# Performance work log

Hardware: AMD Instinct MI355X
Metric: run time of the kernel (lower is better)

## Reference

```python
import jax, jax.numpy as jnp
import numpy as np

N = 100000   # nodes
E = 3200000  # edges
D = 16       # n_qubits / feature dim
H = 64       # classifier hidden
C = 10       # output_dims
L = 2        # len(q_depths)


def setup_inputs() -> dict:
    key = jax.random.key(0)
    ks = jax.random.split(key, 16)
    s = 1.0 / np.sqrt(D)
    return {
        "x": jax.random.normal(ks[0], (N, D), jnp.float32),
        "edge_index": jax.random.randint(ks[1], (2, E), 0, N, dtype=jnp.int32),
        "edge_attr": jax.random.uniform(ks[2], (E,), jnp.float32),
        "batch": jnp.zeros((N,), jnp.int32),
        # per-layer GCNConv params
        "lin_w": jax.random.uniform(ks[3], (L, D, D), jnp.float32, -s, s),
        "conv_b": jnp.zeros((L, D), jnp.float32),
        # per-layer nodeNN (stand-in for quantum_net): tanh(W x + b)
        "node_w": jax.random.uniform(ks[4], (L, D, D), jnp.float32, -s, s),
        "node_b": jnp.zeros((L, D), jnp.float32),
        # per-layer LayerNorm affine
        "ln_g": jnp.ones((L, D), jnp.float32),
        "ln_b": jnp.zeros((L, D), jnp.float32),
        # classifier
        "w1": jax.random.normal(ks[5], (H, D), jnp.float32) * np.sqrt(2.0 / (D + H)),
        "b1": jnp.zeros((H,), jnp.float32),
        "w2": jax.random.normal(ks[6], (C, H), jnp.float32) * np.sqrt(2.0 / (H + C)),
        "b2": jnp.zeros((C,), jnp.float32),
    }


def _layer_norm(h, g, b, eps=1e-5):
    mu = h.mean(-1, keepdims=True)
    var = ((h - mu) ** 2).mean(-1, keepdims=True)
    return (h - mu) * jax.lax.rsqrt(var + eps) * g + b


def reference(x, edge_index, edge_attr, batch, lin_w, conv_b, node_w, node_b,
              ln_g, ln_b, w1, b1, w2, b2):
    n = x.shape[0]
    # gcn_norm with add_self_loops=True (fill_value=1)
    loop = jnp.arange(n, dtype=edge_index.dtype)
    row = jnp.concatenate([edge_index[0], loop])  # source
    col = jnp.concatenate([edge_index[1], loop])  # target
    ew = jnp.concatenate([edge_attr, jnp.ones((n,), x.dtype)])
    deg = jax.ops.segment_sum(ew, col, num_segments=n)
    dinv = jnp.where(deg > 0, jax.lax.rsqrt(jnp.maximum(deg, 1e-30)), 0.0)
    norm = dinv[row] * ew * dinv[col]  # [E+N]

    h = x
    n_layers = lin_w.shape[0]
    for i in range(n_layers):
        out = h @ lin_w[i].T                      # lin (no bias)
        msg = norm[:, None] * out[row]            # gather + scale, [E+N, D]
        agg = jax.ops.segment_sum(msg, col, num_segments=n)  # scatter-add
        out = jnp.tanh(agg @ node_w[i].T + node_b[i])  # nodeNN update (quantum_net stand-in)
        out = out + conv_b[i]
        h = jnp.where(out > 0, out, 0.2 * out)    # LeakyReLU(0.2)
        h = _layer_norm(h, ln_g[i], ln_b[i])

    h = jax.nn.relu(h @ w1.T + b1)                # classifier (dropout = identity at eval)
    return h @ w2.T + b2
```

## Files before the change

kernel.cpp:

```cpp
#include <hip/hip_runtime.h>
#include <hip/hip_bf16.h>

namespace {

constexpr int N_NODES = 100000;
constexpr int N_EDGES = 3200000;
constexpr int D = 16;
constexpr int H = 64;
constexpr int C = 10;
constexpr int L = 2;
constexpr int BLK = 256;
constexpr int BLKS = 512;
constexpr int NBN = (N_NODES + BLK - 1) / BLK;

constexpr int PA = 32;
constexpr int NP = (N_NODES + PA - 1) / PA;

constexpr int CBN = 256;
constexpr int NC = (N_NODES + CBN - 1) / CBN;
constexpr int NPTR = NC * CBN + 1;

constexpr int NBB = 1024;
constexpr int EC = N_EDGES / NBB;
constexpr int REC2_CAP = N_EDGES + 7 * N_NODES;

__device__ inline unsigned short f2bf(float f) {
  unsigned u = __float_as_uint(f);
  return (unsigned short)((u + 0x7FFFu + ((u >> 16) & 1u)) >> 16);
}
__device__ inline float bf2f(unsigned short b) {
  return __uint_as_float(((unsigned)b) << 16);
}

__global__ void k_bincount(const int* __restrict__ col, int* __restrict__ blk_hist) {
  __shared__ int lh[NC];
  for (int i = threadIdx.x; i < NC; i += BLKS) lh[i] = 0;
  __syncthreads();
  const int b = blockIdx.x;
  const int e0 = b * EC, e1 = e0 + EC;
  for (int e = e0 + threadIdx.x; e < e1; e += 4 * BLKS) {
    int cc[4]; bool ok[4];
#pragma unroll
    for (int j = 0; j < 4; ++j) {
      int ee = e + j * BLKS;
      ok[j] = ee < e1;
      cc[j] = ok[j] ? col[ee] : 0;
    }
#pragma unroll
    for (int j = 0; j < 4; ++j)
      if (ok[j]) atomicAdd(&lh[cc[j] >> 8], 1);
  }
  __syncthreads();
  for (int i = threadIdx.x; i < NC; i += BLKS)
    blk_hist[(size_t)b * NC + i] = lh[i];
}

__global__ void k_colscan(int* __restrict__ blk_hist, int* __restrict__ bin_cnt) {
  const int i = blockIdx.x;
  const int t = threadIdx.x;
  int v[4];
  int s = 0;
#pragma unroll
  for (int j = 0; j < 4; ++j) {
    v[j] = blk_hist[(size_t)(t * 4 + j) * NC + i];
    s += v[j];
  }
  const int lane = t & 63;
  int incl = s;
#pragma unroll
  for (int off = 1; off < 64; off <<= 1) {
    int y = __shfl_up(incl, off, 64);
    if (lane >= off) incl += y;
  }
  __shared__ int wsum[4];
  const int w = t >> 6;
  if (lane == 63) wsum[w] = incl;
  __syncthreads();
  int wbase = 0;
#pragma unroll
  for (int k = 0; k < 4; ++k) wbase += (k < w) ? wsum[k] : 0;
  int excl = wbase + incl - s;
#pragma unroll
  for (int j = 0; j < 4; ++j) {
    blk_hist[(size_t)(t * 4 + j) * NC + i] = excl;
    excl += v[j];
  }
  if (t == BLK - 1) bin_cnt[i] = excl;
}

__global__ void k_scan(const int* __restrict__ src, int* __restrict__ dst, int n,
                       int sentinel) {
  __shared__ int s0[2048], s1[2048];
  const int t = threadIdx.x;
  int v0 = (t < n) ? src[t] : 0;
  int v1 = (t + 1024 < n) ? src[t + 1024] : 0;
  s0[t] = v0; s0[t + 1024] = v1;
  __syncthreads();
  int* cur = s0; int* nxt = s1;
  for (int off = 1; off < 2048; off <<= 1) {
    nxt[t] = cur[t] + (t >= off ? cur[t - off] : 0);
    int i1 = t + 1024;
    nxt[i1] = cur[i1] + (i1 >= off ? cur[i1 - off] : 0);
    __syncthreads();
    int* tmp = cur; cur = nxt; nxt = tmp;
  }
  if (t < n) dst[t] = cur[t] - v0;
  if (t + 1024 < n) dst[t + 1024] = cur[t + 1024] - v1;
  if (t == 0 && sentinel >= 0) dst[n] = sentinel;
}

__global__ void k_binscatter(const int* __restrict__ row, const int* __restrict__ col,
                             const float* __restrict__ ew, const int* __restrict__ coarse_ptr,
                             const int* __restrict__ blk_hist, uint2* __restrict__ recs) {
  __shared__ int lcur[NC];
  const int b = blockIdx.x;
  for (int i = threadIdx.x; i < NC; i += BLKS)
    lcur[i] = coarse_ptr[i] + blk_hist[(size_t)b * NC + i];
  __syncthreads();
  const int e0 = b * EC, e1 = e0 + EC;
  for (int e = e0 + threadIdx.x; e < e1; e += 8 * BLKS) {
    int cc[8], rr[8]; float ww[8]; bool ok[8];
#pragma unroll
    for (int j = 0; j < 8; ++j) {
      int ee = e + j * BLKS;
      ok[j] = ee < e1;
      cc[j] = ok[j] ? col[ee] : 0;
      rr[j] = ok[j] ? row[ee] : 0;
      ww[j] = ok[j] ? ew[ee] : 0.f;
    }
#pragma unroll
    for (int j = 0; j < 8; ++j) {
      if (ok[j]) {
        int c = cc[j];
        int pos = atomicAdd(&lcur[c >> 8], 1);
        recs[pos] = make_uint2((unsigned)rr[j] | ((unsigned)(c & (CBN - 1)) << 17),
                               __float_as_uint(ww[j]));
      }
    }
  }
}

__global__ void k_cntnode(const uint2* __restrict__ recs, const int* __restrict__ coarse_ptr,
                          int* __restrict__ cnt_g, int* __restrict__ pad_cnt) {
  __shared__ int cnt[CBN];
  __shared__ int ws[4];
  const int b = blockIdx.x;
  const int tid = threadIdx.x;
  if (tid < CBN) cnt[tid] = 0;
  __syncthreads();
  const int beg = coarse_ptr[b], end = coarse_ptr[b + 1];
  for (int p = beg + tid; p < end; p += 4 * BLKS) {
    unsigned xx[4]; bool ok[4];
#pragma unroll
    for (int j = 0; j < 4; ++j) {
      int pp = p + j * BLKS;
      ok[j] = pp < end;
      xx[j] = ok[j] ? recs[pp].x : 0u;
    }
#pragma unroll
    for (int j = 0; j < 4; ++j)
      if (ok[j]) atomicAdd(&cnt[xx[j] >> 17], 1);
  }
  __syncthreads();
  if (tid < CBN) {
    int c = cnt[tid];
    cnt_g[b * CBN + tid] = c;
    int pv = (c + 7) & ~7;
#pragma unroll
    for (int m = 1; m < 64; m <<= 1) pv += __shfl_xor(pv, m, 64);
    if ((tid & 63) == 0) ws[tid >> 6] = pv;
  }
  __syncthreads();
  if (tid == 0) pad_cnt[b] = ws[0] + ws[1] + ws[2] + ws[3];
}

__global__ void k_sortscatter(const uint2* __restrict__ recs, const int* __restrict__ coarse_ptr,
                              const int* __restrict__ cnt_g, const int* __restrict__ pad_ptr,
                              int* __restrict__ node_ptr, uint2* __restrict__ recs2) {
  __shared__ int cur[CBN];
  __shared__ int fin[CBN];
  __shared__ int wsum[4];
  const int b = blockIdx.x;
  const int tid = threadIdx.x;
  int pc = 0, incl = 0;
  if (tid < CBN) {
    pc = (cnt_g[b * CBN + tid] + 7) & ~7;
    incl = pc;
    const int lane = tid & 63;
#pragma unroll
    for (int off = 1; off < 64; off <<= 1) {
      int y = __shfl_up(incl, off, 64);
      if (lane >= off) incl += y;
    }
    if (lane == 63) wsum[tid >> 6] = incl;
  }
  __syncthreads();
  if (tid < CBN) {
    const int w = tid >> 6;
    int wb = 0;
#pragma unroll
    for (int k = 0; k < 4; ++k) wb += (k < w) ? wsum[k] : 0;
    int excl = wb + incl - pc + pad_ptr[b];
    cur[tid] = excl;
    fin[tid] = excl + pc;
    node_ptr[b * CBN + tid] = excl;
    if (b == NC - 1 && tid == CBN - 1) node_ptr[NC * CBN] = excl + pc;
  }
  __syncthreads();
  const int beg = coarse_ptr[b], end = coarse_ptr[b + 1];
  for (int p = beg + tid; p < end; p += 4 * BLKS) {
    uint2 r[4]; bool ok[4];
#pragma unroll
    for (int j = 0; j < 4; ++j) {
      int pp = p + j * BLKS;
      ok[j] = pp < end;
      r[j] = ok[j] ? recs[pp] : make_uint2(0u, 0u);
    }
#pragma unroll
    for (int j = 0; j < 4; ++j) {
      if (ok[j]) {
        int pos = atomicAdd(&cur[r[j].x >> 17], 1);
        recs2[pos] = make_uint2(r[j].x & 0x1FFFF, r[j].y);
      }
    }
  }
  __syncthreads();
  if (tid < CBN) {
    for (int q = cur[tid]; q < fin[tid]; ++q) recs2[q] = make_uint2(0u, 0u);
  }
}

__global__ void k_dinv2(const int* __restrict__ node_ptr, const uint2* __restrict__ recs2,
                        float* __restrict__ dinv) {
  int v = blockIdx.x * BLK + threadIdx.x;
  if (v >= N_NODES) return;
  float s = 1.0f;
  int e = node_ptr[v + 1];
  for (int p = node_ptr[v]; p < e; ++p) s += __uint_as_float(recs2[p].y);
  dinv[v] = s > 0.f ? rsqrtf(fmaxf(s, 1e-30f)) : 0.f;
}

__global__ void k_lin(const float* __restrict__ hin, const float* __restrict__ W,
                      const float* __restrict__ dinv, unsigned short* __restrict__ outd) {
  __shared__ float sW[D * D];
  sW[threadIdx.x] = W[threadIdx.x];
  __syncthreads();
  int v = blockIdx.x * BLK + threadIdx.x;
  if (v >= N_NODES) return;
  float hv[D];
  const float4* hp = reinterpret_cast<const float4*>(hin + (size_t)v * D);
#pragma unroll
  for (int c = 0; c < 4; ++c) {
    float4 t = hp[c];
    hv[4 * c + 0] = t.x; hv[4 * c + 1] = t.y;
    hv[4 * c + 2] = t.z; hv[4 * c + 3] = t.w;
  }
  float dv = dinv[v];
  unsigned short ob[D];
#pragma unroll
  for (int j = 0; j < D; ++j) {
    float s = 0.f;
#pragma unroll
    for (int k = 0; k < D; ++k) s += hv[k] * sW[j * D + k];
    ob[j] = f2bf(s * dv);
  }
  uint4 w0, w1;
  w0.x = (unsigned)ob[0]  | ((unsigned)ob[1]  << 16);
  w0.y = (unsigned)ob[2]  | ((unsigned)ob[3]  << 16);
  w0.z = (unsigned)ob[4]  | ((unsigned)ob[5]  << 16);
  w0.w = (unsigned)ob[6]  | ((unsigned)ob[7]  << 16);
  w1.x = (unsigned)ob[8]  | ((unsigned)ob[9]  << 16);
  w1.y = (unsigned)ob[10] | ((unsigned)ob[11] << 16);
  w1.z = (unsigned)ob[12] | ((unsigned)ob[13] << 16);
  w1.w = (unsigned)ob[14] | ((unsigned)ob[15] << 16);
  uint4* op = reinterpret_cast<uint4*>(outd + (size_t)v * D);
  op[0] = w0;
  op[1] = w1;
}

__global__ void k_agg(const int* __restrict__ node_ptr, const uint2* __restrict__ recs2,
                      const float* __restrict__ dinv, const unsigned short* __restrict__ outd,
                      const float* __restrict__ Wn, const float* __restrict__ nb,
                      const float* __restrict__ cb, const float* __restrict__ lg,
                      const float* __restrict__ lb, float* __restrict__ h) {
  __shared__ float sacc[PA * 17];
  __shared__ float sdinv[PA];
  __shared__ float sWT[D * D];
  __shared__ float snb[D], scb[D], slg[D], slb[D];
  const int b = blockIdx.x;
  const int base = b * PA;
  const int tid = threadIdx.x;

  sWT[tid] = Wn[(tid & 15) * D + (tid >> 4)];
  if (tid < D) {
    snb[tid] = nb[tid]; scb[tid] = cb[tid];
    slg[tid] = lg[tid]; slb[tid] = lb[tid];
  }
  if (tid < PA) {
    int v = base + tid;
    sdinv[tid] = (v < N_NODES) ? dinv[v] : 0.f;
  }

  const int g = tid >> 4;
  const int l = tid & 15;
#pragma unroll
  for (int i = 0; i < PA / 16; ++i) {
    const int n = g + 16 * i;
    const int v = base + n;
    float acc = (v < N_NODES) ? bf2f(outd[(size_t)v * D + l]) : 0.f;
    int p = node_ptr[v];
    const int e = node_ptr[v + 1];
    uint4 a0, a1, a2, a3;
    if (p < e) {
      const uint4* rp = reinterpret_cast<const uint4*>(recs2 + p);
      a0 = rp[0]; a1 = rp[1]; a2 = rp[2]; a3 = rp[3];
    }
    for (; p < e; p += 8) {
      const int pn = (p + 8 < e) ? p + 8 : p;
      const uint4* rpn = reinterpret_cast<const uint4*>(recs2 + pn);
      uint4 b0 = rpn[0], b1 = rpn[1], b2 = rpn[2], b3 = rpn[3];
      float g0 = bf2f(outd[(size_t)a0.x * D + l]);
      float g1 = bf2f(outd[(size_t)a0.z * D + l]);
      float g2 = bf2f(outd[(size_t)a1.x * D + l]);
      float g3 = bf2f(outd[(size_t)a1.z * D + l]);
      float g4 = bf2f(outd[(size_t)a2.x * D + l]);
      float g5 = bf2f(outd[(size_t)a2.z * D + l]);
      float g6 = bf2f(outd[(size_t)a3.x * D + l]);
      float g7 = bf2f(outd[(size_t)a3.z * D + l]);
      acc = fmaf(__uint_as_float(a0.y), g0, acc);
      acc = fmaf(__uint_as_float(a0.w), g1, acc);
      acc = fmaf(__uint_as_float(a1.y), g2, acc);
      acc = fmaf(__uint_as_float(a1.w), g3, acc);
      acc = fmaf(__uint_as_float(a2.y), g4, acc);
      acc = fmaf(__uint_as_float(a2.w), g5, acc);
      acc = fmaf(__uint_as_float(a3.y), g6, acc);
      acc = fmaf(__uint_as_float(a3.w), g7, acc);
      a0 = b0; a1 = b1; a2 = b2; a3 = b3;
    }
    sacc[n * 17 + l] = acc;
  }
  __syncthreads();

#pragma unroll
  for (int nb0 = 0; nb0 < PA / 16; ++nb0) {
    int n = nb0 * 16 + g;
    int v = base + n;
    float s = 0.f;
#pragma unroll
    for (int k = 0; k < D; ++k) s += sacc[n * 17 + k] * sWT[k * D + l];
    s = snb[l] + sdinv[n] * s;
    float u = tanhf(s) + scb[l];
    u = u > 0.f ? u : 0.2f * u;
    float mu = u;
#pragma unroll
    for (int m = 1; m < 16; m <<= 1) mu += __shfl_xor(mu, m, 64);
    mu *= (1.0f / D);
    float dd = u - mu;
    float var = dd * dd;
#pragma unroll
    for (int m = 1; m < 16; m <<= 1) var += __shfl_xor(var, m, 64);
    var *= (1.0f / D);
    float inv = rsqrtf(var + 1e-5f);
    if (v < N_NODES) h[(size_t)v * D + l] = dd * inv * slg[l] + slb[l];
  }
}

__global__ void k_cls(const float* __restrict__ h, const float* __restrict__ w1,
                      const float* __restrict__ b1, const float* __restrict__ w2,
                      const float* __restrict__ b2, float* __restrict__ out) {
  __shared__ float sw1[H * D];
  __shared__ float sb1[H];
  __shared__ float sw2[C * H];
  __shared__ float sb2[C];
  for (int i = threadIdx.x; i < H * D; i += BLK) sw1[i] = w1[i];
  for (int i = threadIdx.x; i < H; i += BLK) sb1[i] = b1[i];
  for (int i = threadIdx.x; i < C * H; i += BLK) sw2[i] = w2[i];
  for (int i = threadIdx.x; i < C; i += BLK) sb2[i] = b2[i];
  __syncthreads();
  int v = blockIdx.x * BLK + threadIdx.x;
  if (v >= N_NODES) return;
  float hv[D];
  const float4* hp = reinterpret_cast<const float4*>(h + (size_t)v * D);
#pragma unroll
  for (int c = 0; c < 4; ++c) {
    float4 t = hp[c];
    hv[4 * c + 0] = t.x; hv[4 * c + 1] = t.y;
    hv[4 * c + 2] = t.z; hv[4 * c + 3] = t.w;
  }
  float oc[C];
#pragma unroll
  for (int c = 0; c < C; ++c) oc[c] = sb2[c];
#pragma unroll
  for (int j = 0; j < H; ++j) {
    float s = sb1[j];
#pragma unroll
    for (int k = 0; k < D; ++k) s += hv[k] * sw1[j * D + k];
    s = fmaxf(s, 0.f);
#pragma unroll
    for (int c = 0; c < C; ++c) oc[c] += s * sw2[c * H + j];
  }
#pragma unroll
  for (int c = 0; c < C; ++c) out[(size_t)v * C + c] = oc[c];
}

inline char* align_up(char* p, size_t a) {
  return (char*)(((uintptr_t)p + a - 1) & ~(uintptr_t)(a - 1));
}

}

extern "C" void kernel_launch(void* const* d_in, const int* in_sizes, int n_in,
                              void* d_out, int out_size, void* d_ws, size_t ws_size,
                              hipStream_t stream) {
  const float* x         = (const float*)d_in[0];
  const int*   edge_idx  = (const int*)d_in[1];
  const float* edge_attr = (const float*)d_in[2];
  const float* lin_w  = (const float*)d_in[4];
  const float* conv_b = (const float*)d_in[5];
  const float* node_w = (const float*)d_in[6];
  const float* node_b = (const float*)d_in[7];
  const float* ln_g   = (const float*)d_in[8];
  const float* ln_b   = (const float*)d_in[9];
  const float* w1     = (const float*)d_in[10];
  const float* b1     = (const float*)d_in[11];
  const float* w2     = (const float*)d_in[12];
  const float* b2     = (const float*)d_in[13];
  float* out = (float*)d_out;

  const int* row = edge_idx;
  const int* col = edge_idx + N_EDGES;

  char* p = (char*)d_ws;
  int*   bin_cnt    = (int*)p;   p = align_up(p + sizeof(int) * NC, 256);
  int*   coarse_ptr = (int*)p;   p = align_up(p + sizeof(int) * (NC + 1), 256);
  int*   pad_cnt    = (int*)p;   p = align_up(p + sizeof(int) * NC, 256);
  int*   pad_ptr    = (int*)p;   p = align_up(p + sizeof(int) * (NC + 1), 256);
  int*   cnt_g      = (int*)p;   p = align_up(p + sizeof(int) * (size_t)(NC * CBN), 256);
  int*   node_ptr   = (int*)p;   p = align_up(p + sizeof(int) * (size_t)NPTR, 256);
  float* dinv       = (float*)p; p = align_up(p + sizeof(float) * N_NODES, 256);
  char*  recs_mem   = p;         p = align_up(p + sizeof(uint2) * (size_t)N_EDGES, 256);
  uint2* recs2      = (uint2*)p; p = align_up(p + sizeof(uint2) * (size_t)REC2_CAP, 256);

  uint2* recs = (uint2*)recs_mem;
  unsigned short* outb = (unsigned short*)recs_mem;
  float* hbuf = (float*)align_up(recs_mem + sizeof(unsigned short) * (size_t)N_NODES * D, 256);
  int*   blk_hist = (int*)recs2;

  k_bincount<<<NBB, BLKS, 0, stream>>>(col, blk_hist);
  k_colscan<<<NC, BLK, 0, stream>>>(blk_hist, bin_cnt);
  k_scan<<<1, 1024, 0, stream>>>(bin_cnt, coarse_ptr, NC, N_EDGES);
  k_binscatter<<<NBB, BLKS, 0, stream>>>(row, col, edge_attr, coarse_ptr, blk_hist, recs);
  k_cntnode<<<NC, BLKS, 0, stream>>>(recs, coarse_ptr, cnt_g, pad_cnt);
  k_scan<<<1, 1024, 0, stream>>>(pad_cnt, pad_ptr, NC, -1);
  k_sortscatter<<<NC, BLKS, 0, stream>>>(recs, coarse_ptr, cnt_g, pad_ptr, node_ptr, recs2);
  k_dinv2<<<NBN, BLK, 0, stream>>>(node_ptr, recs2, dinv);

  for (int i = 0; i < L; ++i) {
    const float* hin = (i == 0) ? x : hbuf;
    k_lin<<<NBN, BLK, 0, stream>>>(hin, lin_w + i * D * D, dinv, outb);
    k_agg<<<NP, BLK, 0, stream>>>(node_ptr, recs2, dinv, outb,
                                  node_w + i * D * D, node_b + i * D, conv_b + i * D,
                                  ln_g + i * D, ln_b + i * D, hbuf);
  }
  k_cls<<<NBN, BLK, 0, stream>>>(hbuf, w1, b1, w2, b2, out);
}
```

Before: 194.5 us.

## Fuse next-layer linear and classifier into aggregation kernel epilogues

Measured after the change: 192.7 us. About the same (-0.9%).

```diff
diff --git a/kernel.cpp b/kernel.cpp
--- a/kernel.cpp
+++ b/kernel.cpp
@@ -8,7 +8,6 @@
 constexpr int D = 16;
 constexpr int H = 64;
 constexpr int C = 10;
-constexpr int L = 2;
 constexpr int BLK = 256;
 constexpr int BLKS = 512;
 constexpr int NBN = (N_NODES + BLK - 1) / BLK;
@@ -278,15 +277,26 @@
   op[1] = w1;
 }
 
+template <int MODE>
 __global__ void k_agg(const int* __restrict__ node_ptr, const uint2* __restrict__ recs2,
                       const float* __restrict__ dinv, const unsigned short* __restrict__ outd,
                       const float* __restrict__ Wn, const float* __restrict__ nb,
                       const float* __restrict__ cb, const float* __restrict__ lg,
-                      const float* __restrict__ lb, float* __restrict__ h) {
+                      const float* __restrict__ lb,
+                      const float* __restrict__ Wlin_next,
+                      unsigned short* __restrict__ outd_next,
+                      const float* __restrict__ w1, const float* __restrict__ b1,
+                      const float* __restrict__ w2, const float* __restrict__ b2,
+                      float* __restrict__ outc) {
   __shared__ float sacc[PA * 17];
   __shared__ float sdinv[PA];
   __shared__ float sWT[D * D];
   __shared__ float snb[D], scb[D], slg[D], slb[D];
+  __shared__ float sWT2[D * D];
+  __shared__ float sw1[H * D];
+  __shared__ float sb1[H];
+  __shared__ float sw2[C * H];
+  __shared__ float sb2[C];
   const int b = blockIdx.x;
   const int base = b * PA;
   const int tid = threadIdx.x;
@@ -296,10 +306,20 @@
     snb[tid] = nb[tid]; scb[tid] = cb[tid];
     slg[tid] = lg[tid]; slb[tid] = lb[tid];
   }
+  if constexpr (MODE == 1) {
+    sWT2[tid] = Wlin_next[(tid & 15) * D + (tid >> 4)];
+  }
+  if constexpr (MODE == 2) {
+    for (int i = tid; i < H * D; i += BLK) sw1[i] = w1[i];
+    if (tid < H) sb1[tid] = b1[tid];
+    for (int i = tid; i < C * H; i += BLK) sw2[i] = w2[i];
+    if (tid < C) sb2[tid] = b2[tid];
+  }
   if (tid < PA) {
     int v = base + tid;
     sdinv[tid] = (v < N_NODES) ? dinv[v] : 0.f;
   }
+  __syncthreads();
 
   const int g = tid >> 4;
   const int l = tid & 15;
@@ -318,7 +338,7 @@
     for (; p < e; p += 8) {
       const int pn = (p + 8 < e) ? p + 8 : p;
       const uint4* rpn = reinterpret_cast<const uint4*>(recs2 + pn);
-      uint4 b0 = rpn[0], b1 = rpn[1], b2 = rpn[2], b3 = rpn[3];
+      uint4 b0 = rpn[0], b1_ = rpn[1], b2_ = rpn[2], b3 = rpn[3];
       float g0 = bf2f(outd[(size_t)a0.x * D + l]);
       float g1 = bf2f(outd[(size_t)a0.z * D + l]);
       float g2 = bf2f(outd[(size_t)a1.x * D + l]);
@@ -335,7 +355,7 @@
       acc = fmaf(__uint_as_float(a2.w), g5, acc);
       acc = fmaf(__uint_as_float(a3.y), g6, acc);
       acc = fmaf(__uint_as_float(a3.w), g7, acc);
-      a0 = b0; a1 = b1; a2 = b2; a3 = b3;
+      a0 = b0; a1 = b1_; a2 = b2_; a3 = b3;
     }
     sacc[n * 17 + l] = acc;
   }
@@ -361,46 +381,40 @@
     for (int m = 1; m < 16; m <<= 1) var += __shfl_xor(var, m, 64);
     var *= (1.0f / D);
     float inv = rsqrtf(var + 1e-5f);
-    if (v < N_NODES) h[(size_t)v * D + l] = dd * inv * slg[l] + slb[l];
-  }
-}
-
-__global__ void k_cls(const float* __restrict__ h, const float* __restrict__ w1,
-                      const float* __restrict__ b1, const float* __restrict__ w2,
-                      const float* __restrict__ b2, float* __restrict__ out) {
-  __shared__ float sw1[H * D];
-  __shared__ float sb1[H];
-  __shared__ float sw2[C * H];
-  __shared__ float sb2[C];
-  for (int i = threadIdx.x; i < H * D; i += BLK) sw1[i] = w1[i];
-  for (int i = threadIdx.x; i < H; i += BLK) sb1[i] = b1[i];
-  for (int i = threadIdx.x; i < C * H; i += BLK) sw2[i] = w2[i];
-  for (int i = threadIdx.x; i < C; i += BLK) sb2[i] = b2[i];
-  __syncthreads();
-  int v = blockIdx.x * BLK + threadIdx.x;
-  if (v >= N_NODES) return;
-  float hv[D];
-  const float4* hp = reinterpret_cast<const float4*>(h + (size_t)v * D);
-#pragma unroll
-  for (int c = 0; c < 4; ++c) {
-    float4 t = hp[c];
-    hv[4 * c + 0] = t.x; hv[4 * c + 1] = t.y;
-    hv[4 * c + 2] = t.z; hv[4 * c + 3] = t.w;
-  }
-  float oc[C];
-#pragma unroll
-  for (int c = 0; c < C; ++c) oc[c] = sb2[c];
-#pragma unroll
-  for (int j = 0; j < H; ++j) {
-    float s = sb1[j];
-#pragma unroll
-    for (int k = 0; k < D; ++k) s += hv[k] * sw1[j * D + k];
-    s = fmaxf(s, 0.f);
-#pragma unroll
-    for (int c = 0; c < C; ++c) oc[c] += s * sw2[c * H + j];
-  }
-#pragma unroll
-  for (int c = 0; c < C; ++c) out[(size_t)v * C + c] = oc[c];
+    float hval = dd * inv * slg[l] + slb[l];
+
+    sacc[n * 17 + l] = hval;
+
+    if constexpr (MODE == 1) {
+      float s2 = 0.f;
+#pragma unroll
+      for (int k = 0; k < D; ++k) s2 += sacc[n * 17 + k] * sWT2[k * D + l];
+      if (v < N_NODES) outd_next[(size_t)v * D + l] = f2bf(s2 * sdinv[n]);
+    } else {
+      float po[C];
+#pragma unroll
+      for (int c = 0; c < C; ++c) po[c] = 0.f;
+#pragma unroll
+      for (int jj = 0; jj < 4; ++jj) {
+        int j = l + 16 * jj;
+        float t = sb1[j];
+#pragma unroll
+        for (int k = 0; k < D; ++k) t += sacc[n * 17 + k] * sw1[j * D + k];
+        t = fmaxf(t, 0.f);
+#pragma unroll
+        for (int c = 0; c < C; ++c) po[c] += t * sw2[c * H + j];
+      }
+#pragma unroll
+      for (int m = 1; m < 16; m <<= 1) {
+#pragma unroll
+        for (int c = 0; c < C; ++c) po[c] += __shfl_xor(po[c], m, 64);
+      }
+      float sel = 0.f;
+#pragma unroll
+      for (int c = 0; c < C; ++c) sel = (l == c) ? po[c] : sel;
+      if (v < N_NODES && l < C) outc[(size_t)v * C + l] = sel + sb2[l];
+    }
+  }
 }
 
 inline char* align_up(char* p, size_t a) {
@@ -442,9 +456,10 @@
   uint2* recs2      = (uint2*)p; p = align_up(p + sizeof(uint2) * (size_t)REC2_CAP, 256);
 
   uint2* recs = (uint2*)recs_mem;
-  unsigned short* outb = (unsigned short*)recs_mem;
-  float* hbuf = (float*)align_up(recs_mem + sizeof(unsigned short) * (size_t)N_NODES * D, 256);
-  int*   blk_hist = (int*)recs2;
+  unsigned short* outbA = (unsigned short*)recs_mem;
+  unsigned short* outbB = (unsigned short*)align_up(
+      recs_mem + sizeof(unsigned short) * (size_t)N_NODES * D, 256);
+  int* blk_hist = (int*)recs2;
 
   k_bincount<<<NBB, BLKS, 0, stream>>>(col, blk_hist);
   k_colscan<<<NC, BLK, 0, stream>>>(blk_hist, bin_cnt);
@@ -455,12 +470,14 @@
   k_sortscatter<<<NC, BLKS, 0, stream>>>(recs, coarse_ptr, cnt_g, pad_ptr, node_ptr, recs2);
   k_dinv2<<<NBN, BLK, 0, stream>>>(node_ptr, recs2, dinv);
 
-  for (int i = 0; i < L; ++i) {
-    const float* hin = (i == 0) ? x : hbuf;
-    k_lin<<<NBN, BLK, 0, stream>>>(hin, lin_w + i * D * D, dinv, outb);
-    k_agg<<<NP, BLK, 0, stream>>>(node_ptr, recs2, dinv, outb,
-                                  node_w + i * D * D, node_b + i * D, conv_b + i * D,
-                                  ln_g + i * D, ln_b + i * D, hbuf);
-  }
-  k_cls<<<NBN, BLK, 0, stream>>>(hbuf, w1, b1, w2, b2, out);
-}
+  k_lin<<<NBN, BLK, 0, stream>>>(x, lin_w, dinv, outbA);
+  k_agg<1><<<NP, BLK, 0, stream>>>(node_ptr, recs2, dinv, outbA,
+                                   node_w, node_b, conv_b, ln_g, ln_b,
+                                   lin_w + D * D, outbB,
+                                   nullptr, nullptr, nullptr, nullptr, nullptr);
+  k_agg<2><<<NP, BLK, 0, stream>>>(node_ptr, recs2, dinv, outbB,
+                                   node_w + D * D, node_b + D, conv_b + D,
+                                   ln_g + D, ln_b + D,
+                                   nullptr, nullptr,
+                                   w1, b1, w2, b2, out);
+}
```
